# Performance work log

Hardware: AMD Instinct MI355X
Metric: run time of the kernel (lower is better)

Reference implementation:

```python
import jax, jax.numpy as jnp
import numpy as np

T, B, F_, H, D, C = 16, 1024, 512, 128, 8, 100  # trees, batch, feat, hidden, depth, classes
L = 2 ** (D + 1)  # n_leaf = 512


def _routing_tables():
    # Static per-leaf routing: node index and branch side at each depth.
    # Derived from compute_mu's gather indices:
    #   node(d, l) = 2^d - 1 + l // 2^(D+1-d);  side(d, l) = (l // 2^(D-d)) % 2
    l = np.arange(L)
    node = np.stack([(2 ** d - 1) + l // (2 ** (D + 1 - d)) for d in range(D + 1)])  # [D+1, L]
    side = np.stack([(l // (2 ** (D - d))) % 2 for d in range(D + 1)])               # [D+1, L]
    return jnp.asarray(node, dtype=jnp.int32), jnp.asarray(side.astype(np.bool_))


def setup_inputs() -> dict:
    key = jax.random.key(0)
    ks = jax.random.split(key, 4)
    return {
        "feat": jax.random.normal(ks[0], (B, F_), jnp.float32),
        "W1": jax.random.normal(ks[1], (T, F_, H), jnp.float32) * 0.05,
        "b1": jnp.zeros((T, H), jnp.float32),
        "W2": jax.random.normal(ks[2], (T, H, L), jnp.float32) * 0.05,
        "b2": jnp.zeros((T, L), jnp.float32),
        "pi": jax.random.uniform(ks[3], (T, L, C), jnp.float32, -2.0, 2.0),
    }


def reference(feat, W1, b1, W2, b2, pi):
    node, side = _routing_tables()
    # Per-tree MLP head (dropout is identity in eval mode).
    h = jax.nn.relu(jnp.einsum('bf,tfh->tbh', feat, W1) + b1[:, None, :])        # [T,B,H]
    p = jax.nn.sigmoid(jnp.einsum('tbh,thl->tbl', h, W2) + b2[:, None, :])       # [T,B,L]
    # compute_mu: product of routing probs along each root->leaf path.
    sel = p[:, :, node]                          # [T,B,D+1,L] gather (static indices)
    route = jnp.where(side, 1.0 - sel, sel)      # left -> p, right -> 1-p
    mu = jnp.prod(route, axis=2)                 # [T,B,L]
    # compute_py_x: mean over leaves then mean over trees of mu @ softmax(pi).
    leaf_p = jax.nn.softmax(pi, axis=-1)         # [T,L,C]
    py_x = jnp.einsum('tbl,tlc->bc', mu, leaf_p) / (L * T)  # [B,C]
    return jnp.log(py_x)
```

## Files before the change

### kernel.cpp

```cpp
#include <hip/hip_runtime.h>
#include <hip/hip_bf16.h>
#include <math.h>

#define T_ 16
#define B_ 1024
#define F_ 512
#define H_ 128
#define D_ 8
#define C_ 100
#define L_ 512
#define CP_ 112

typedef __attribute__((ext_vector_type(8))) short bf16x8_t;
typedef __attribute__((ext_vector_type(4))) float f32x4_t;

__device__ inline ushort f2bf(float x) {
  __hip_bfloat16 b = __float2bfloat16(x);
  return *(ushort*)&b;
}
__device__ inline float bf2f(ushort u) {
  union { unsigned int i; float f; } v;
  v.i = ((unsigned int)u) << 16;
  return v.f;
}

__global__ __launch_bounds__(256) void k_prep(
    const float* __restrict__ feat, const float* __restrict__ W1,
    const float* __restrict__ W2, const float* __restrict__ pi,
    ushort* __restrict__ feat_bf, ushort* __restrict__ W1T,
    ushort* __restrict__ W2T, ushort* __restrict__ lpT) {
  __shared__ ushort ubuf[112 * 48];
  float (*tile)[33] = (float(*)[33])ubuf;
  ushort (*tileT)[48] = (ushort(*)[48])ubuf;
  const int bid = blockIdx.x, tid = threadIdx.x;

  if (bid < 256) {
    int i = (bid * 256 + tid) * 8;
    float4 a = *(const float4*)(feat + i);
    float4 b = *(const float4*)(feat + i + 4);
    bf16x8_t o;
    o[0] = (short)f2bf(a.x); o[1] = (short)f2bf(a.y);
    o[2] = (short)f2bf(a.z); o[3] = (short)f2bf(a.w);
    o[4] = (short)f2bf(b.x); o[5] = (short)f2bf(b.y);
    o[6] = (short)f2bf(b.z); o[7] = (short)f2bf(b.w);
    *(bf16x8_t*)(feat_bf + i) = o;
    return;
  }
  if (bid < 2304) {
    const float* X; ushort* XT; int K, N, kb, nb, s;
    if (bid < 1280) {
      int r = bid - 256;  kb = r & 15; nb = (r >> 4) & 3;  s = r >> 6;
      X = W1; XT = W1T; K = F_; N = H_;
    } else {
      int r = bid - 1280; kb = r & 3;  nb = (r >> 2) & 15; s = r >> 6;
      X = W2; XT = W2T; K = H_; N = L_;
    }
    const int k0 = kb * 32, n0 = nb * 32;
    const int c = tid & 31, r0 = tid >> 5;
    const float* Xs = X + (size_t)s * K * N;
    ushort* XTs = XT + (size_t)s * N * K;
#pragma unroll
    for (int j = 0; j < 4; ++j)
      tile[r0 + 8 * j][c] = Xs[(size_t)(k0 + r0 + 8 * j) * N + n0 + c];
    __syncthreads();
#pragma unroll
    for (int j = 0; j < 4; ++j)
      XTs[(size_t)(n0 + r0 + 8 * j) * K + k0 + c] = f2bf(tile[c][r0 + 8 * j]);
    return;
  }
  {
    int bid2 = bid - 2304;
    int t = bid2 >> 4, l0 = (bid2 & 15) << 5;
    int lane = tid & 63;
#pragma unroll
    for (int p = 0; p < 8; ++p) {
      int rl = p * 4 + (tid >> 6);
      const float* x = pi + (size_t)(t * L_ + l0 + rl) * C_;
      float v0 = (lane < C_) ? x[lane] : -1e30f;
      float v1 = (lane + 64 < C_) ? x[lane + 64] : -1e30f;
      float m = fmaxf(v0, v1);
#pragma unroll
      for (int off = 32; off; off >>= 1) m = fmaxf(m, __shfl_xor(m, off, 64));
      float e0 = __expf(v0 - m);
      float e1 = (lane + 64 < C_) ? __expf(v1 - m) : 0.0f;
      float sm = e0 + e1;
#pragma unroll
      for (int off = 32; off; off >>= 1) sm += __shfl_xor(sm, off, 64);
      float inv = 1.0f / sm;
      if (lane < C_) tileT[lane][rl] = f2bf(e0 * inv);
      int c2 = lane + 64;
      if (c2 < CP_) tileT[c2][rl] = f2bf(c2 < C_ ? e1 * inv : 0.0f);
    }
    __syncthreads();
    ushort* dst = lpT + (size_t)t * CP_ * L_ + l0;
    for (int idx = tid; idx < 448; idx += 256) {
      int c = idx >> 2, ch = (idx & 3) * 8;
      *(bf16x8_t*)(dst + (size_t)c * L_ + ch) = *(const bf16x8_t*)&tileT[c][ch];
    }
  }
}

__global__ __launch_bounds__(256) void k12_mfma(
    const ushort* __restrict__ feat, const ushort* __restrict__ W1T,
    const float* __restrict__ b1, const ushort* __restrict__ W2T,
    const float* __restrict__ b2, const ushort* __restrict__ lpT,
    float* __restrict__ part) {
  __shared__ ushort smem[29696];
  ushort (*h_s)[136] = (ushort(*)[136])smem;
  ushort (*a_s)[72]  = (ushort(*)[72])(smem + 4352);
  ushort (*b_s)[72]  = (ushort(*)[72])(smem + 6656);
  ushort (*w_s)[136] = (ushort(*)[136])(smem + 4352);
  ushort (*p_s)[520] = (ushort(*)[520])(smem + 13056);

  const int bid = blockIdx.x;
  const int t = bid & 15, b0 = (bid >> 4) * 32;
  const int tid = threadIdx.x;
  const int w = tid >> 6, lane = tid & 63, quad = lane >> 4, n = lane & 15;

  {
    f32x4_t acc[2][2];
#pragma unroll
    for (int i = 0; i < 2; ++i)
#pragma unroll
      for (int j = 0; j < 2; ++j) acc[i][j] = (f32x4_t){0.f, 0.f, 0.f, 0.f};

    for (int kc = 0; kc < 8; ++kc) {
      __syncthreads();
      {
        int row = tid >> 3, col8 = (tid & 7) * 8;
        *(bf16x8_t*)&a_s[row][col8] =
            *(const bf16x8_t*)(feat + (size_t)(b0 + row) * F_ + kc * 64 + col8);
      }
#pragma unroll
      for (int i = 0; i < 4; ++i) {
        int idx = i * 256 + tid;
        int row = idx >> 3, col8 = (idx & 7) * 8;
        *(bf16x8_t*)&b_s[row][col8] =
            *(const bf16x8_t*)(W1T + ((size_t)t * H_ + row) * F_ + kc * 64 + col8);
      }
      __syncthreads();
#pragma unroll
      for (int ks = 0; ks < 64; ks += 32) {
        bf16x8_t af[2], bfr[2];
#pragma unroll
        for (int mt = 0; mt < 2; ++mt)
          af[mt] = *(const bf16x8_t*)&a_s[mt * 16 + n][ks + quad * 8];
#pragma unroll
        for (int nt = 0; nt < 2; ++nt)
          bfr[nt] = *(const bf16x8_t*)&b_s[w * 32 + nt * 16 + n][ks + quad * 8];
#pragma unroll
        for (int mt = 0; mt < 2; ++mt)
#pragma unroll
          for (int nt = 0; nt < 2; ++nt)
            acc[mt][nt] = __builtin_amdgcn_mfma_f32_16x16x32_bf16(
                af[mt], bfr[nt], acc[mt][nt], 0, 0, 0);
      }
    }
    float bias[2] = {b1[t * H_ + w * 32 + n], b1[t * H_ + w * 32 + 16 + n]};
#pragma unroll
    for (int mt = 0; mt < 2; ++mt)
#pragma unroll
      for (int nt = 0; nt < 2; ++nt)
#pragma unroll
        for (int r = 0; r < 4; ++r) {
          int row = mt * 16 + quad * 4 + r;
          int col = w * 32 + nt * 16 + n;
          float v = acc[mt][nt][r] + bias[nt];
          h_s[row][col] = f2bf(v > 0.f ? v : 0.f);
        }
  }
  __syncthreads();

  {
    bf16x8_t af2[2][4];
#pragma unroll
    for (int mt = 0; mt < 2; ++mt)
#pragma unroll
      for (int ks = 0; ks < 4; ++ks)
        af2[mt][ks] = *(const bf16x8_t*)&h_s[mt * 16 + n][ks * 32 + quad * 8];

    for (int nc = 0; nc < 8; ++nc) {
      __syncthreads();
#pragma unroll
      for (int i = 0; i < 4; ++i) {
        int idx = i * 256 + tid;
        int row = idx >> 4, col8 = (idx & 15) * 8;
        *(bf16x8_t*)&w_s[row][col8] =
            *(const bf16x8_t*)(W2T + ((size_t)t * L_ + nc * 64 + row) * H_ + col8);
      }
      __syncthreads();
      f32x4_t acc[2];
      acc[0] = (f32x4_t){0.f, 0.f, 0.f, 0.f};
      acc[1] = (f32x4_t){0.f, 0.f, 0.f, 0.f};
#pragma unroll
      for (int ks = 0; ks < 4; ++ks) {
        bf16x8_t bfrag = *(const bf16x8_t*)&w_s[w * 16 + n][ks * 32 + quad * 8];
        acc[0] = __builtin_amdgcn_mfma_f32_16x16x32_bf16(af2[0][ks], bfrag,
                                                         acc[0], 0, 0, 0);
        acc[1] = __builtin_amdgcn_mfma_f32_16x16x32_bf16(af2[1][ks], bfrag,
                                                         acc[1], 0, 0, 0);
      }
      int l = nc * 64 + w * 16 + n;
      float bias = b2[t * L_ + l];
#pragma unroll
      for (int mt = 0; mt < 2; ++mt)
#pragma unroll
        for (int r = 0; r < 4; ++r) {
          float x = acc[mt][r] + bias;
          p_s[mt * 16 + quad * 4 + r][l] = f2bf(1.0f / (1.0f + __expf(-x)));
        }
    }
  }
  __syncthreads();

  bf16x8_t mo[4][2];
#pragma unroll
  for (int pass = 0; pass < 4; ++pass) {
    int b = pass * 8 + (tid >> 5);
    int s = tid & 31;
    float P = 1.f;
#pragma unroll
    for (int d = 0; d < 5; ++d) {
      int nd = (1 << d) - 1 + (s >> (5 - d));
      int sd = (s >> (4 - d)) & 1;
      float pv = bf2f(p_s[b][nd]);
      P *= sd ? (1.f - pv) : pv;
    }
    float p5 = bf2f(p_s[b][31 + s]);
    float q5[2] = {P * p5, P * (1.f - p5)};
    float q6[4], q7[8];
#pragma unroll
    for (int j = 0; j < 2; ++j) {
      float pv = bf2f(p_s[b][63 + 2 * s + j]);
      q6[2 * j] = q5[j] * pv;
      q6[2 * j + 1] = q5[j] * (1.f - pv);
    }
#pragma unroll
    for (int u = 0; u < 4; ++u) {
      float pv = bf2f(p_s[b][127 + 4 * s + u]);
      q7[2 * u] = q6[u] * pv;
      q7[2 * u + 1] = q6[u] * (1.f - pv);
    }
    bf16x8_t o0, o1;
#pragma unroll
    for (int v = 0; v < 8; ++v) {
      float pv = bf2f(p_s[b][255 + 8 * s + v]);
      ushort e0 = f2bf(q7[v] * pv);
      ushort e1 = f2bf(q7[v] * (1.f - pv));
      if (v < 4) { o0[2 * v] = (short)e0; o0[2 * v + 1] = (short)e1; }
      else       { o1[2 * (v - 4)] = (short)e0; o1[2 * (v - 4) + 1] = (short)e1; }
    }
    mo[pass][0] = o0;
    mo[pass][1] = o1;
  }
  __syncthreads();
#pragma unroll
  for (int pass = 0; pass < 4; ++pass) {
    int b = pass * 8 + (tid >> 5);
    int s = tid & 31;
    *(bf16x8_t*)&p_s[b][s * 16]     = mo[pass][0];
    *(bf16x8_t*)&p_s[b][s * 16 + 8] = mo[pass][1];
  }
  __syncthreads();

  {
    const int mt = w >> 1;
    const int nt0 = (w & 1) * 4;
    const int ncnt = (w & 1) ? 3 : 4;
    const ushort* arow = &p_s[mt * 16 + n][0];
    const ushort* brow = lpT + (size_t)t * CP_ * L_ +
                         ((size_t)(nt0 * 16 + n)) * L_ + quad * 8;
    f32x4_t acc[4];
#pragma unroll
    for (int i = 0; i < 4; ++i) acc[i] = (f32x4_t){0.f, 0.f, 0.f, 0.f};
#pragma unroll 4
    for (int k = 0; k < L_; k += 32) {
      bf16x8_t af = *(const bf16x8_t*)(arow + k + quad * 8);
#pragma unroll
      for (int j = 0; j < 4; ++j) {
        if (j < ncnt) {
          bf16x8_t bfr = *(const bf16x8_t*)(brow + (size_t)j * 16 * L_ + k);
          acc[j] = __builtin_amdgcn_mfma_f32_16x16x32_bf16(af, bfr, acc[j],
                                                           0, 0, 0);
        }
      }
    }
    const int m0 = b0 + mt * 16 + quad * 4;
#pragma unroll
    for (int j = 0; j < 4; ++j) {
      int c = (nt0 + j) * 16 + n;
      if (j < ncnt && c < C_) {
#pragma unroll
        for (int r = 0; r < 4; ++r)
          part[((size_t)t * B_ + m0 + r) * C_ + c] = acc[j][r];
      }
    }
  }
}

__global__ __launch_bounds__(256) void k6_log(
    const float* __restrict__ part, float* __restrict__ out) {
  int i = blockIdx.x * 256 + threadIdx.x;
  if (i < B_ * C_) {
    float s = 0.0f;
#pragma unroll
    for (int t = 0; t < T_; ++t) s += part[(size_t)t * B_ * C_ + i];
    out[i] = logf(s * (1.0f / (L_ * T_)));
  }
}

extern "C" void kernel_launch(void* const* d_in, const int* in_sizes, int n_in,
                              void* d_out, int out_size, void* d_ws,
                              size_t ws_size, hipStream_t stream) {
  const float* feat = (const float*)d_in[0];
  const float* W1   = (const float*)d_in[1];
  const float* b1   = (const float*)d_in[2];
  const float* W2   = (const float*)d_in[3];
  const float* b2   = (const float*)d_in[4];
  const float* pi   = (const float*)d_in[5];
  float* out = (float*)d_out;

  char* ws = (char*)d_ws;
  ushort* feat_bf  = (ushort*)(ws);
  ushort* W1T_buf  = (ushort*)(ws + ((size_t)1 << 20));
  ushort* W2T_buf  = (ushort*)(ws + ((size_t)3 << 20));
  ushort* lpT_buf  = (ushort*)(ws + ((size_t)5 << 20));
  float*  part_buf = (float*)(ws + ((size_t)7 << 20));

  k_prep<<<2560, 256, 0, stream>>>(feat, W1, W2, pi, feat_bf, W1T_buf,
                                   W2T_buf, lpT_buf);
  k12_mfma<<<512, 256, 0, stream>>>(feat_bf, W1T_buf, b1, W2T_buf, b2,
                                    lpT_buf, part_buf);
  k6_log<<<(B_ * C_ + 255) / 256, 256, 0, stream>>>(part_buf, out);
}
```

Measured before the change: 115.0 us.

## Halve batch tile per block to double grid size and raise occupancy

```diff
diff --git a/kernel.cpp b/kernel.cpp
--- a/kernel.cpp
+++ b/kernel.cpp
@@ -100,33 +100,31 @@
   }
 }
 
-__global__ __launch_bounds__(256) void k12_mfma(
+__global__ __launch_bounds__(256, 4) void k12_mfma(
     const ushort* __restrict__ feat, const ushort* __restrict__ W1T,
     const float* __restrict__ b1, const ushort* __restrict__ W2T,
     const float* __restrict__ b2, const ushort* __restrict__ lpT,
     float* __restrict__ part) {
-  __shared__ ushort smem[29696];
-  ushort (*h_s)[136] = (ushort(*)[136])smem;
-  ushort (*a_s)[72]  = (ushort(*)[72])(smem + 4352);
-  ushort (*b_s)[72]  = (ushort(*)[72])(smem + 6656);
-  ushort (*w_s)[136] = (ushort(*)[136])(smem + 4352);
-  ushort (*p_s)[520] = (ushort(*)[520])(smem + 13056);
+  __shared__ ushort smem[20288];
+  ushort (*a_s)[68]  = (ushort(*)[68])smem;
+  ushort (*b_s)[68]  = (ushort(*)[68])(smem + 1088);
+  ushort (*w_s)[136] = (ushort(*)[136])smem;
+  ushort (*h_s)[136] = (ushort(*)[136])(smem + 9792);
+  ushort (*p_s)[520] = (ushort(*)[520])(smem + 11968);
 
   const int bid = blockIdx.x;
-  const int t = bid & 15, b0 = (bid >> 4) * 32;
+  const int t = bid & 15, b0 = (bid >> 4) * 16;
   const int tid = threadIdx.x;
   const int w = tid >> 6, lane = tid & 63, quad = lane >> 4, n = lane & 15;
 
   {
-    f32x4_t acc[2][2];
-#pragma unroll
-    for (int i = 0; i < 2; ++i)
-#pragma unroll
-      for (int j = 0; j < 2; ++j) acc[i][j] = (f32x4_t){0.f, 0.f, 0.f, 0.f};
+    f32x4_t acc[2];
+    acc[0] = (f32x4_t){0.f, 0.f, 0.f, 0.f};
+    acc[1] = (f32x4_t){0.f, 0.f, 0.f, 0.f};
 
     for (int kc = 0; kc < 8; ++kc) {
       __syncthreads();
-      {
+      if (tid < 128) {
         int row = tid >> 3, col8 = (tid & 7) * 8;
         *(bf16x8_t*)&a_s[row][col8] =
             *(const bf16x8_t*)(feat + (size_t)(b0 + row) * F_ + kc * 64 + col8);
@@ -141,43 +139,31 @@
       __syncthreads();
 #pragma unroll
       for (int ks = 0; ks < 64; ks += 32) {
-        bf16x8_t af[2], bfr[2];
-#pragma unroll
-        for (int mt = 0; mt < 2; ++mt)
-          af[mt] = *(const bf16x8_t*)&a_s[mt * 16 + n][ks + quad * 8];
-#pragma unroll
-        for (int nt = 0; nt < 2; ++nt)
-          bfr[nt] = *(const bf16x8_t*)&b_s[w * 32 + nt * 16 + n][ks + quad * 8];
-#pragma unroll
-        for (int mt = 0; mt < 2; ++mt)
-#pragma unroll
-          for (int nt = 0; nt < 2; ++nt)
-            acc[mt][nt] = __builtin_amdgcn_mfma_f32_16x16x32_bf16(
-                af[mt], bfr[nt], acc[mt][nt], 0, 0, 0);
+        bf16x8_t af = *(const bf16x8_t*)&a_s[n][ks + quad * 8];
+        bf16x8_t bfr0 = *(const bf16x8_t*)&b_s[w * 32 + n][ks + quad * 8];
+        bf16x8_t bfr1 = *(const bf16x8_t*)&b_s[w * 32 + 16 + n][ks + quad * 8];
+        acc[0] = __builtin_amdgcn_mfma_f32_16x16x32_bf16(af, bfr0, acc[0],
+                                                         0, 0, 0);
+        acc[1] = __builtin_amdgcn_mfma_f32_16x16x32_bf16(af, bfr1, acc[1],
+                                                         0, 0, 0);
       }
     }
     float bias[2] = {b1[t * H_ + w * 32 + n], b1[t * H_ + w * 32 + 16 + n]};
 #pragma unroll
-    for (int mt = 0; mt < 2; ++mt)
-#pragma unroll
-      for (int nt = 0; nt < 2; ++nt)
-#pragma unroll
-        for (int r = 0; r < 4; ++r) {
-          int row = mt * 16 + quad * 4 + r;
-          int col = w * 32 + nt * 16 + n;
-          float v = acc[mt][nt][r] + bias[nt];
-          h_s[row][col] = f2bf(v > 0.f ? v : 0.f);
-        }
+    for (int nt = 0; nt < 2; ++nt)
+#pragma unroll
+      for (int r = 0; r < 4; ++r) {
+        float v = acc[nt][r] + bias[nt];
+        h_s[quad * 4 + r][w * 32 + nt * 16 + n] = f2bf(v > 0.f ? v : 0.f);
+      }
   }
   __syncthreads();
 
   {
-    bf16x8_t af2[2][4];
-#pragma unroll
-    for (int mt = 0; mt < 2; ++mt)
-#pragma unroll
-      for (int ks = 0; ks < 4; ++ks)
-        af2[mt][ks] = *(const bf16x8_t*)&h_s[mt * 16 + n][ks * 32 + quad * 8];
+    bf16x8_t af2[4];
+#pragma unroll
+    for (int ks = 0; ks < 4; ++ks)
+      af2[ks] = *(const bf16x8_t*)&h_s[n][ks * 32 + quad * 8];
 
     for (int nc = 0; nc < 8; ++nc) {
       __syncthreads();
@@ -189,33 +175,27 @@
             *(const bf16x8_t*)(W2T + ((size_t)t * L_ + nc * 64 + row) * H_ + col8);
       }
       __syncthreads();
-      f32x4_t acc[2];
-      acc[0] = (f32x4_t){0.f, 0.f, 0.f, 0.f};
-      acc[1] = (f32x4_t){0.f, 0.f, 0.f, 0.f};
+      f32x4_t acc = (f32x4_t){0.f, 0.f, 0.f, 0.f};
 #pragma unroll
       for (int ks = 0; ks < 4; ++ks) {
         bf16x8_t bfrag = *(const bf16x8_t*)&w_s[w * 16 + n][ks * 32 + quad * 8];
-        acc[0] = __builtin_amdgcn_mfma_f32_16x16x32_bf16(af2[0][ks], bfrag,
-                                                         acc[0], 0, 0, 0);
-        acc[1] = __builtin_amdgcn_mfma_f32_16x16x32_bf16(af2[1][ks], bfrag,
-                                                         acc[1], 0, 0, 0);
+        acc = __builtin_amdgcn_mfma_f32_16x16x32_bf16(af2[ks], bfrag, acc,
+                                                      0, 0, 0);
       }
       int l = nc * 64 + w * 16 + n;
       float bias = b2[t * L_ + l];
 #pragma unroll
-      for (int mt = 0; mt < 2; ++mt)
-#pragma unroll
-        for (int r = 0; r < 4; ++r) {
-          float x = acc[mt][r] + bias;
-          p_s[mt * 16 + quad * 4 + r][l] = f2bf(1.0f / (1.0f + __expf(-x)));
-        }
+      for (int r = 0; r < 4; ++r) {
+        float x = acc[r] + bias;
+        p_s[quad * 4 + r][l] = f2bf(1.0f / (1.0f + __expf(-x)));
+      }
     }
   }
   __syncthreads();
 
-  bf16x8_t mo[4][2];
-#pragma unroll
-  for (int pass = 0; pass < 4; ++pass) {
+  bf16x8_t mo[2][2];
+#pragma unroll
+  for (int pass = 0; pass < 2; ++pass) {
     int b = pass * 8 + (tid >> 5);
     int s = tid & 31;
     float P = 1.f;
@@ -255,7 +235,7 @@
   }
   __syncthreads();
 #pragma unroll
-  for (int pass = 0; pass < 4; ++pass) {
+  for (int pass = 0; pass < 2; ++pass) {
     int b = pass * 8 + (tid >> 5);
     int s = tid & 31;
     *(bf16x8_t*)&p_s[b][s * 16]     = mo[pass][0];
@@ -264,20 +244,19 @@
   __syncthreads();
 
   {
-    const int mt = w >> 1;
-    const int nt0 = (w & 1) * 4;
-    const int ncnt = (w & 1) ? 3 : 4;
-    const ushort* arow = &p_s[mt * 16 + n][0];
+    const int nt0 = w * 2;
+    const int ncnt = (w == 3) ? 1 : 2;
+    const ushort* arow = &p_s[n][0];
     const ushort* brow = lpT + (size_t)t * CP_ * L_ +
                          ((size_t)(nt0 * 16 + n)) * L_ + quad * 8;
-    f32x4_t acc[4];
-#pragma unroll
-    for (int i = 0; i < 4; ++i) acc[i] = (f32x4_t){0.f, 0.f, 0.f, 0.f};
+    f32x4_t acc[2];
+    acc[0] = (f32x4_t){0.f, 0.f, 0.f, 0.f};
+    acc[1] = (f32x4_t){0.f, 0.f, 0.f, 0.f};
 #pragma unroll 4
     for (int k = 0; k < L_; k += 32) {
       bf16x8_t af = *(const bf16x8_t*)(arow + k + quad * 8);
 #pragma unroll
-      for (int j = 0; j < 4; ++j) {
+      for (int j = 0; j < 2; ++j) {
         if (j < ncnt) {
           bf16x8_t bfr = *(const bf16x8_t*)(brow + (size_t)j * 16 * L_ + k);
           acc[j] = __builtin_amdgcn_mfma_f32_16x16x32_bf16(af, bfr, acc[j],
@@ -285,9 +264,9 @@
         }
       }
     }
-    const int m0 = b0 + mt * 16 + quad * 4;
-#pragma unroll
-    for (int j = 0; j < 4; ++j) {
+    const int m0 = b0 + quad * 4;
+#pragma unroll
+    for (int j = 0; j < 2; ++j) {
       int c = (nt0 + j) * 16 + n;
       if (j < ncnt && c < C_) {
 #pragma unroll
@@ -329,7 +308,7 @@
 
   k_prep<<<2560, 256, 0, stream>>>(feat, W1, W2, pi, feat_bf, W1T_buf,
                                    W2T_buf, lpT_buf);
-  k12_mfma<<<512, 256, 0, stream>>>(feat_bf, W1T_buf, b1, W2T_buf, b2,
-                                    lpT_buf, part_buf);
+  k12_mfma<<<1024, 256, 0, stream>>>(feat_bf, W1T_buf, b1, W2T_buf, b2,
+                                     lpT_buf, part_buf);
   k6_log<<<(B_ * C_ + 255) / 256, 256, 0, stream>>>(part_buf, out);
 }
```

Result: slower. 132.3 us (+15.1%).

## Prefetch next K/N chunk into registers to overlap global loads with MFMA

Applied to the files above, without the earlier changes.

```diff
diff --git a/kernel.cpp b/kernel.cpp
--- a/kernel.cpp
+++ b/kernel.cpp
@@ -117,6 +117,10 @@
   const int tid = threadIdx.x;
   const int w = tid >> 6, lane = tid & 63, quad = lane >> 4, n = lane & 15;
 
+  const int arow = tid >> 3, acol = (tid & 7) * 8;
+  const ushort* featp = feat + (size_t)(b0 + arow) * F_ + acol;
+  const ushort* w1p   = W1T + ((size_t)t * H_ + arow) * F_ + acol;
+
   {
     f32x4_t acc[2][2];
 #pragma unroll
@@ -124,21 +128,23 @@
 #pragma unroll
       for (int j = 0; j < 2; ++j) acc[i][j] = (f32x4_t){0.f, 0.f, 0.f, 0.f};
 
+    bf16x8_t ra, rb[4];
+    ra = *(const bf16x8_t*)(featp);
+#pragma unroll
+    for (int i = 0; i < 4; ++i)
+      rb[i] = *(const bf16x8_t*)(w1p + (size_t)i * 32 * F_);
+    *(bf16x8_t*)&a_s[arow][acol] = ra;
+#pragma unroll
+    for (int i = 0; i < 4; ++i)
+      *(bf16x8_t*)&b_s[i * 32 + arow][acol] = rb[i];
+    __syncthreads();
+    ra = *(const bf16x8_t*)(featp + 64);
+#pragma unroll
+    for (int i = 0; i < 4; ++i)
+      rb[i] = *(const bf16x8_t*)(w1p + (size_t)i * 32 * F_ + 64);
+
+#pragma unroll
     for (int kc = 0; kc < 8; ++kc) {
-      __syncthreads();
-      {
-        int row = tid >> 3, col8 = (tid & 7) * 8;
-        *(bf16x8_t*)&a_s[row][col8] =
-            *(const bf16x8_t*)(feat + (size_t)(b0 + row) * F_ + kc * 64 + col8);
-      }
-#pragma unroll
-      for (int i = 0; i < 4; ++i) {
-        int idx = i * 256 + tid;
-        int row = idx >> 3, col8 = (idx & 7) * 8;
-        *(bf16x8_t*)&b_s[row][col8] =
-            *(const bf16x8_t*)(W1T + ((size_t)t * H_ + row) * F_ + kc * 64 + col8);
-      }
-      __syncthreads();
 #pragma unroll
       for (int ks = 0; ks < 64; ks += 32) {
         bf16x8_t af[2], bfr[2];
@@ -154,6 +160,20 @@
           for (int nt = 0; nt < 2; ++nt)
             acc[mt][nt] = __builtin_amdgcn_mfma_f32_16x16x32_bf16(
                 af[mt], bfr[nt], acc[mt][nt], 0, 0, 0);
+      }
+      __syncthreads();
+      if (kc < 7) {
+        *(bf16x8_t*)&a_s[arow][acol] = ra;
+#pragma unroll
+        for (int i = 0; i < 4; ++i)
+          *(bf16x8_t*)&b_s[i * 32 + arow][acol] = rb[i];
+        __syncthreads();
+        if (kc < 6) {
+          ra = *(const bf16x8_t*)(featp + (kc + 2) * 64);
+#pragma unroll
+          for (int i = 0; i < 4; ++i)
+            rb[i] = *(const bf16x8_t*)(w1p + (size_t)i * 32 * F_ + (kc + 2) * 64);
+        }
       }
     }
     float bias[2] = {b1[t * H_ + w * 32 + n], b1[t * H_ + w * 32 + 16 + n]};
@@ -169,26 +189,32 @@
           h_s[row][col] = f2bf(v > 0.f ? v : 0.f);
         }
   }
-  __syncthreads();
 
   {
+    const int wrow = tid >> 4, wcol = (tid & 15) * 8;
+    const ushort* w2p = W2T + ((size_t)t * L_ + wrow) * H_ + wcol;
+    bf16x8_t rw[4];
+#pragma unroll
+    for (int i = 0; i < 4; ++i)
+      rw[i] = *(const bf16x8_t*)(w2p + (size_t)(i * 16) * H_);
+    __syncthreads();
+
     bf16x8_t af2[2][4];
 #pragma unroll
     for (int mt = 0; mt < 2; ++mt)
 #pragma unroll
       for (int ks = 0; ks < 4; ++ks)
         af2[mt][ks] = *(const bf16x8_t*)&h_s[mt * 16 + n][ks * 32 + quad * 8];
-
+#pragma unroll
+    for (int i = 0; i < 4; ++i)
+      *(bf16x8_t*)&w_s[i * 16 + wrow][wcol] = rw[i];
+    __syncthreads();
+#pragma unroll
+    for (int i = 0; i < 4; ++i)
+      rw[i] = *(const bf16x8_t*)(w2p + (size_t)(64 + i * 16) * H_);
+
+#pragma unroll
     for (int nc = 0; nc < 8; ++nc) {
-      __syncthreads();
-#pragma unroll
-      for (int i = 0; i < 4; ++i) {
-        int idx = i * 256 + tid;
-        int row = idx >> 4, col8 = (idx & 15) * 8;
-        *(bf16x8_t*)&w_s[row][col8] =
-            *(const bf16x8_t*)(W2T + ((size_t)t * L_ + nc * 64 + row) * H_ + col8);
-      }
-      __syncthreads();
       f32x4_t acc[2];
       acc[0] = (f32x4_t){0.f, 0.f, 0.f, 0.f};
       acc[1] = (f32x4_t){0.f, 0.f, 0.f, 0.f};
@@ -209,6 +235,18 @@
           float x = acc[mt][r] + bias;
           p_s[mt * 16 + quad * 4 + r][l] = f2bf(1.0f / (1.0f + __expf(-x)));
         }
+      __syncthreads();
+      if (nc < 7) {
+#pragma unroll
+        for (int i = 0; i < 4; ++i)
+          *(bf16x8_t*)&w_s[i * 16 + wrow][wcol] = rw[i];
+        __syncthreads();
+        if (nc < 6) {
+#pragma unroll
+          for (int i = 0; i < 4; ++i)
+            rw[i] = *(const bf16x8_t*)(w2p + (size_t)((nc + 2) * 64 + i * 16) * H_);
+        }
+      }
     }
   }
   __syncthreads();
@@ -267,7 +305,7 @@
     const int mt = w >> 1;
     const int nt0 = (w & 1) * 4;
     const int ncnt = (w & 1) ? 3 : 4;
-    const ushort* arow = &p_s[mt * 16 + n][0];
+    const ushort* arow2 = &p_s[mt * 16 + n][0];
     const ushort* brow = lpT + (size_t)t * CP_ * L_ +
                          ((size_t)(nt0 * 16 + n)) * L_ + quad * 8;
     f32x4_t acc[4];
@@ -275,7 +313,7 @@
     for (int i = 0; i < 4; ++i) acc[i] = (f32x4_t){0.f, 0.f, 0.f, 0.f};
 #pragma unroll 4
     for (int k = 0; k < L_; k += 32) {
-      bf16x8_t af = *(const bf16x8_t*)(arow + k + quad * 8);
+      bf16x8_t af = *(const bf16x8_t*)(arow2 + k + quad * 8);
 #pragma unroll
       for (int j = 0; j < 4; ++j) {
         if (j < ncnt) {
```

After: 110.5 us. -3.8%, faster.
